# Performance work log

Hardware: AMD Instinct MI355X
Metric: run time of the kernel (lower is better)

## Reference

```python
import jax, jax.numpy as jnp
import numpy as np

N_NODES = 100000


def gcn_conv(x, W, b, src, dst, n):
    # PyG GCNConv: linear transform, add self-loops, symmetric degree norm, scatter-add, bias
    h = x @ W                                      # [n, d_out]
    loop = jnp.arange(n, dtype=src.dtype)
    s = jnp.concatenate([src, loop])               # [E + n]
    d = jnp.concatenate([dst, loop])
    deg = jax.ops.segment_sum(jnp.ones_like(d, dtype=h.dtype), d, num_segments=n)
    dinv = jnp.where(deg > 0, jax.lax.rsqrt(deg), 0.0)
    norm = dinv[s] * dinv[d]                       # [E + n]
    msg = h[s] * norm[:, None]                     # gather + scale
    out = jax.ops.segment_sum(msg, d, num_segments=n)  # scatter-add over targets
    return out + b


def setup_inputs() -> dict:
    key = jax.random.key(0)
    ks = jax.random.split(key, 8)
    n, c_in, hid, c_out = N_NODES, 256, 128, 64
    x = jax.random.normal(ks[0], (n, c_in), dtype=jnp.float32)
    edge_index = jax.random.randint(ks[1], (2, 1600000), 0, n, dtype=jnp.int64)
    s = 0.1
    return {
        "x": x,
        "edge_index": edge_index,
        "W1": jax.random.normal(ks[2], (c_in, hid), dtype=jnp.float32) * s,
        "b1": jnp.zeros((hid,), dtype=jnp.float32),
        "Wmu": jax.random.normal(ks[3], (hid, c_out), dtype=jnp.float32) * s,
        "bmu": jnp.zeros((c_out,), dtype=jnp.float32),
        "Wlv": jax.random.normal(ks[4], (hid, c_out), dtype=jnp.float32) * s,
        "blv": jnp.zeros((c_out,), dtype=jnp.float32),
    }


def reference(x, edge_index, W1, b1, Wmu, bmu, Wlv, blv):
    n = x.shape[0]
    src, dst = edge_index[0], edge_index[1]
    h = jax.nn.relu(gcn_conv(x, W1, b1, src, dst, n))
    mu = gcn_conv(h, Wmu, bmu, src, dst, n)
    logvar = gcn_conv(h, Wlv, blv, src, dst, n)
    return mu, logvar
```

## Files before the change

### kernel.cpp

```cpp
#include <hip/hip_runtime.h>


#define C_IN  256
#define HID   128
#define C_OUT 64
#define NBUCK 1024
#define P1WGS 256

typedef __attribute__((ext_vector_type(8))) short bf16x8;
typedef __attribute__((ext_vector_type(4))) float f32x4;

__device__ inline unsigned short f2bf(float f) {
  unsigned u = __float_as_uint(f);
  unsigned r = u + 0x7FFF + ((u >> 16) & 1);
  return (unsigned short)(r >> 16);
}
__device__ inline float bflo(unsigned v) { return __uint_as_float(v << 16); }
__device__ inline float bfhi(unsigned v) { return __uint_as_float(v & 0xFFFF0000u); }

__global__ __launch_bounds__(256) void k_bin_count(const int* __restrict__ dst,
                                                   int* __restrict__ histmat, int E) {
  __shared__ int h[NBUCK];
  int tid = threadIdx.x;
  for (int i = tid; i < NBUCK; i += 256) h[i] = 0;
  __syncthreads();
  for (int e = blockIdx.x * 256 + tid; e < E; e += P1WGS * 256)
    atomicAdd(&h[dst[e] >> 7], 1);
  __syncthreads();
  for (int i = tid; i < NBUCK; i += 256)
    histmat[blockIdx.x * NBUCK + i] = h[i];
}

__global__ __launch_bounds__(256) void k_col_scan(int* __restrict__ histmat,
                                                  int* __restrict__ bucket_tot) {
  __shared__ int sh[P1WGS];
  int b = blockIdx.x;
  int t = threadIdx.x;
  int v = histmat[t * NBUCK + b];
  sh[t] = v; __syncthreads();
  for (int ofs = 1; ofs < P1WGS; ofs <<= 1) {
    int add = (t >= ofs) ? sh[t - ofs] : 0;
    __syncthreads();
    sh[t] += add;
    __syncthreads();
  }
  histmat[t * NBUCK + b] = sh[t] - v;
  if (t == P1WGS - 1) bucket_tot[b] = sh[t];
}

__global__ void k_bucket_scan(const int* __restrict__ bucket_tot,
                              int* __restrict__ bucket_start, int E) {
  __shared__ int sh[NBUCK];
  int t = threadIdx.x;
  int v = bucket_tot[t];
  sh[t] = v; __syncthreads();
  for (int ofs = 1; ofs < NBUCK; ofs <<= 1) {
    int add = (t >= ofs) ? sh[t - ofs] : 0;
    __syncthreads();
    sh[t] += add;
    __syncthreads();
  }
  bucket_start[t] = sh[t] - v;
  if (t == NBUCK - 1) bucket_start[NBUCK] = E;
}

__global__ __launch_bounds__(256) void k_bin_scatter(const int* __restrict__ src,
                                                     const int* __restrict__ dst,
                                                     const int* __restrict__ histmat,
                                                     const int* __restrict__ bucket_start,
                                                     unsigned* __restrict__ binned, int E) {
  __shared__ int cur[NBUCK];
  int tid = threadIdx.x;
  for (int i = tid; i < NBUCK; i += 256)
    cur[i] = bucket_start[i] + histmat[blockIdx.x * NBUCK + i];
  __syncthreads();
  for (int e = blockIdx.x * 256 + tid; e < E; e += P1WGS * 256) {
    int d = dst[e];
    int pos = atomicAdd(&cur[d >> 7], 1);
    binned[pos] = (unsigned)src[e] | ((unsigned)(d & 127) << 17);
  }
}

__global__ __launch_bounds__(256) void k_bucket_csr(const unsigned* __restrict__ binned,
                                                    const int* __restrict__ bucket_start,
                                                    int* __restrict__ row_start,
                                                    float* __restrict__ dinv,
                                                    int* __restrict__ csr_src,
                                                    int n, int E) {
  __shared__ int h[128], ls[128], c[128];
  int b = blockIdx.x, t = threadIdx.x;
  int start = bucket_start[b], end = bucket_start[b + 1];
  if (t < 128) h[t] = 0;
  __syncthreads();
  for (int e = start + t; e < end; e += 256)
    atomicAdd(&h[binned[e] >> 17], 1);
  __syncthreads();
  if (t < 128) ls[t] = h[t];
  __syncthreads();
  for (int ofs = 1; ofs < 128; ofs <<= 1) {
    int add = (t < 128 && t >= ofs) ? ls[t - ofs] : 0;
    __syncthreads();
    if (t < 128) ls[t] += add;
    __syncthreads();
  }
  if (t < 128) {
    int excl = ls[t] - h[t];
    ls[t] = excl;
    c[t] = excl;
    int node = b * 128 + t;
    if (node < n) {
      row_start[node] = start + excl;
      dinv[node] = rsqrtf((float)h[t] + 1.0f);
    }
  }
  if (b == 0 && t == 0) row_start[n] = E;
  __syncthreads();
  for (int e = start + t; e < end; e += 256) {
    unsigned v = binned[e];
    int pos = start + atomicAdd(&c[v >> 17], 1);
    csr_src[pos] = (int)(v & 0x1FFFF);
  }
}

__global__ void k_prep(const float* __restrict__ W1, const float* __restrict__ Wmu,
                       const float* __restrict__ Wlv,
                       unsigned short* __restrict__ bswz1,
                       unsigned short* __restrict__ bswz2) {
  int idx = blockIdx.x * 256 + threadIdx.x;
  if (idx < 4096) {
    int L = idx & 63, t = (idx >> 6) & 7, s = idx >> 9;
    const float* srcp = W1 + (size_t)(s * 32 + ((L >> 4) << 3)) * 128 + t * 16 + (L & 15);
    unsigned short* dstp = bswz1 + (size_t)idx * 8;
#pragma unroll
    for (int j = 0; j < 8; j++) dstp[j] = f2bf(srcp[(size_t)j * 128]);
  } else if (idx < 6144) {
    int id2 = idx - 4096;
    int L = id2 & 63, t = (id2 >> 6) & 7, s = id2 >> 9;
    int nn = t * 16 + (L & 15);
    int k0 = s * 32 + ((L >> 4) << 3);
    const float* W = (nn < C_OUT) ? (Wmu + nn) : (Wlv + (nn - C_OUT));
    unsigned short* dstp = bswz2 + (size_t)id2 * 8;
#pragma unroll
    for (int j = 0; j < 8; j++) dstp[j] = f2bf(W[(size_t)(k0 + j) * C_OUT]);
  }
}

template <typename AT, int K>
__global__ __launch_bounds__(256) void k_gemm_mfma(const AT* __restrict__ A,
                                                   const unsigned short* __restrict__ bswz,
                                                   unsigned short* __restrict__ C,
                                                   int M) {
  constexpr int NS = K / 32;
  int wave = threadIdx.x >> 6, lane = threadIdx.x & 63;
  int m0 = blockIdx.x * 64 + wave * 16;
  int lrow = lane & 15, lq = lane >> 4;
  int arow = m0 + lrow;
  bool rv = arow < M;
  const AT* ap = A + (size_t)(rv ? arow : 0) * K + lq * 8;

  auto loadA = [&](int s) -> bf16x8 {
    if (sizeof(AT) == 4) {
      const float* af = (const float*)ap + s * 32;
      float4 u0 = rv ? *(const float4*)(af) : float4{0, 0, 0, 0};
      float4 u1 = rv ? *(const float4*)(af + 4) : float4{0, 0, 0, 0};
      union { unsigned short us[8]; bf16x8 v; } tmp;
      tmp.us[0] = f2bf(u0.x); tmp.us[1] = f2bf(u0.y);
      tmp.us[2] = f2bf(u0.z); tmp.us[3] = f2bf(u0.w);
      tmp.us[4] = f2bf(u1.x); tmp.us[5] = f2bf(u1.y);
      tmp.us[6] = f2bf(u1.z); tmp.us[7] = f2bf(u1.w);
      return tmp.v;
    } else {
      const unsigned short* ab = (const unsigned short*)ap + s * 32;
      return rv ? *(const bf16x8*)(ab) : (bf16x8)(short)0;
    }
  };

  f32x4 acc[8];
#pragma unroll
  for (int t = 0; t < 8; t++) acc[t] = (f32x4){0.f, 0.f, 0.f, 0.f};

  bf16x8 a_cur = loadA(0);
  bf16x8 b_cur[8];
#pragma unroll
  for (int t = 0; t < 8; t++)
    b_cur[t] = *(const bf16x8*)(bswz + lane * 8 + t * 512);

#pragma unroll
  for (int s = 0; s < NS; ++s) {
    bf16x8 a_nxt = a_cur;
    bf16x8 b_nxt[8];
    if (s + 1 < NS) {
      a_nxt = loadA(s + 1);
      const unsigned short* bp = bswz + (size_t)(s + 1) * 4096 + lane * 8;
#pragma unroll
      for (int t = 0; t < 8; t++) b_nxt[t] = *(const bf16x8*)(bp + t * 512);
    }
#pragma unroll
    for (int t = 0; t < 8; t++)
      acc[t] = __builtin_amdgcn_mfma_f32_16x16x32_bf16(a_cur, b_cur[t], acc[t], 0, 0, 0);
    a_cur = a_nxt;
    if (s + 1 < NS) {
#pragma unroll
      for (int t = 0; t < 8; t++) b_cur[t] = b_nxt[t];
    }
  }
#pragma unroll
  for (int i = 0; i < 4; i++) {
    int rr = m0 + lq * 4 + i;
    if (rr < M) {
      unsigned short* cp = C + (size_t)rr * 128 + lrow;
#pragma unroll
      for (int t = 0; t < 8; t++) cp[t * 16] = f2bf(acc[t][i]);
    }
  }
}

__device__ inline float rdlane_f(float v, int k) {
  return __uint_as_float(__builtin_amdgcn_readlane(__float_as_uint(v), k));
}

#define AGG_BODY                                                                    \
  int wid = (blockIdx.x * blockDim.x + threadIdx.x) >> 6;                           \
  int lane = threadIdx.x & 63;                                                      \
  if (wid >= n) return;                                                             \
  int rs = row_start[wid], re = row_start[wid + 1];                                 \
  float di = dinv[wid];                                                             \
  float acc0 = 0.f, acc1 = 0.f;                                                     \
  for (int base = rs; base < re + 1; base += 64) {                                  \
    int idx = base + lane;                                                          \
    int sl = wid; float wl = 0.f;                                                   \
    if (idx < re) { sl = csr[idx]; wl = dinv[sl]; }                                 \
    else if (idx == re) { wl = di; }                                 \
    int m = re + 1 - base; if (m > 64) m = 64;                                      \
    int mr = (m + 7) & ~7;                                               \
    for (int k = 0; k < mr; k += 8) {                                               \
      _Pragma("unroll")                                                             \
      for (int j = 0; j < 8; j++) {                                                 \
        int kk = k + j;                                                             \
        int sk = __builtin_amdgcn_readlane(sl, kk);                                 \
        float wk = rdlane_f(wl, kk);                                                \
        unsigned v = *(const unsigned*)(p + (size_t)sk * 128 + 2 * lane);           \
        acc0 += bflo(v) * wk;                                                       \
        acc1 += bfhi(v) * wk;                                                       \
      }                                                                             \
    }                                                                               \
  }                                                                                 \
  acc0 *= di; acc1 *= di;

__global__ __launch_bounds__(256) void k_agg_relu_bf(
    const unsigned short* __restrict__ p, const float* __restrict__ dinv,
    const int* __restrict__ row_start, const int* __restrict__ csr,
    const float* __restrict__ bias, unsigned short* __restrict__ h, int n) {
  AGG_BODY
  float2 bb = *(const float2*)(bias + 2 * lane);
  float r0 = fmaxf(acc0 + bb.x, 0.f);
  float r1 = fmaxf(acc1 + bb.y, 0.f);
  unsigned pk = (unsigned)f2bf(r0) | ((unsigned)f2bf(r1) << 16);
  *(unsigned*)(h + (size_t)wid * 128 + 2 * lane) = pk;
}

__global__ __launch_bounds__(256) void k_agg_out_bf(
    const unsigned short* __restrict__ p, const float* __restrict__ dinv,
    const int* __restrict__ row_start, const int* __restrict__ csr,
    const float* __restrict__ bmu, const float* __restrict__ blv,
    float* __restrict__ out, int n) {
  AGG_BODY
  float2 bb = (lane < 32) ? *(const float2*)(bmu + 2 * lane)
                          : *(const float2*)(blv + 2 * lane - 64);
  float* op = (lane < 32) ? (out + (size_t)wid * C_OUT + 2 * lane)
                          : (out + (size_t)(n + wid) * C_OUT + 2 * lane - 64);
  float2 res = {acc0 + bb.x, acc1 + bb.y};
  *(float2*)op = res;
}

extern "C" void kernel_launch(void* const* d_in, const int* in_sizes, int n_in,
                              void* d_out, int out_size, void* d_ws, size_t ws_size,
                              hipStream_t stream) {
  const float* x   = (const float*)d_in[0];
  const int*   ei  = (const int*)d_in[1];
  const float* W1  = (const float*)d_in[2];
  const float* b1  = (const float*)d_in[3];
  const float* Wmu = (const float*)d_in[4];
  const float* bmu = (const float*)d_in[5];
  const float* Wlv = (const float*)d_in[6];
  const float* blv = (const float*)d_in[7];
  float* out = (float*)d_out;

  const int n = in_sizes[0] / C_IN;
  const int E = in_sizes[1] / 2;
  const int* src = ei;
  const int* dst = ei + E;

  char* w = (char*)d_ws;
  auto alloc = [&](size_t bytes) -> void* {
    void* pp = (void*)w;
    w += (bytes + 255) & ~(size_t)255;
    return pp;
  };
  float*          dinv       = (float*)alloc((size_t)n * 4);
  int*            row_start  = (int*)alloc((size_t)(n + 1) * 4);
  int*            histmat    = (int*)alloc((size_t)P1WGS * NBUCK * 4);
  int*            bucket_tot = (int*)alloc((size_t)NBUCK * 4);
  int*            bucket_st  = (int*)alloc((size_t)(NBUCK + 1) * 4);
  unsigned*       binned     = (unsigned*)alloc((size_t)E * 4);
  int*            csr_src    = (int*)alloc((size_t)E * 4);
  unsigned short* bswz1      = (unsigned short*)alloc((size_t)C_IN * 128 * 2);
  unsigned short* bswz2      = (unsigned short*)alloc((size_t)HID * 128 * 2);
  unsigned short* p1         = (unsigned short*)alloc((size_t)n * 128 * 2);
  unsigned short* hbuf       = (unsigned short*)alloc((size_t)n * 128 * 2);
  unsigned short* p2         = (unsigned short*)alloc((size_t)n * 128 * 2);
  (void)ws_size; (void)n_in; (void)out_size;

  const int TB = 256;
  const int gemm_bks = (n + 63) / 64;
  const int agg_bks = (int)(((size_t)n * 64 + TB - 1) / TB);
  const int nbk_csr = (n + 127) / 128;

  k_bin_count<<<P1WGS, TB, 0, stream>>>(dst, histmat, E);
  k_col_scan<<<NBUCK, TB, 0, stream>>>(histmat, bucket_tot);
  k_bucket_scan<<<1, NBUCK, 0, stream>>>(bucket_tot, bucket_st, E);
  k_bin_scatter<<<P1WGS, TB, 0, stream>>>(src, dst, histmat, bucket_st, binned, E);
  k_bucket_csr<<<nbk_csr, TB, 0, stream>>>(binned, bucket_st, row_start, dinv,
                                           csr_src, n, E);

  k_prep<<<24, 256, 0, stream>>>(W1, Wmu, Wlv, bswz1, bswz2);

  k_gemm_mfma<float, C_IN><<<gemm_bks, TB, 0, stream>>>(x, bswz1, p1, n);
  k_agg_relu_bf<<<agg_bks, TB, 0, stream>>>(p1, dinv, row_start, csr_src, b1, hbuf, n);

  k_gemm_mfma<unsigned short, HID><<<gemm_bks, TB, 0, stream>>>(hbuf, bswz2, p2, n);
  k_agg_out_bf<<<agg_bks, TB, 0, stream>>>(p2, dinv, row_start, csr_src, bmu, blv, out, n);
}
```

Measured before the change: 406.1 us.

## Pre-scale GEMM rows by dinv and aggregate over feature slices

The GEMM epilogue now multiplies each output row by dinv[src] and writes it in a sliced layout of 8 slices with 16 columns each, so the aggregation no longer gathers a per-edge weight. Aggregation is split across 8 slice blocks per node group. Within a wave, each 8-lane group handles one edge and reads a 32-byte slice row, and the partial sums are combined with xor shuffles. The intent is a smaller per-slice gather footprint that stays cache-resident and less readlane/scalar overhead. In exchange, the csr lists and row_start are read eight times and each wave does a reduction.

```diff
diff --git a/kernel.cpp b/kernel.cpp
--- a/kernel.cpp
+++ b/kernel.cpp
@@ -105,7 +105,6 @@
   }
   if (t < 128) {
     int excl = ls[t] - h[t];
-    ls[t] = excl;
     c[t] = excl;
     int node = b * 128 + t;
     if (node < n) {
@@ -148,7 +147,8 @@
 template <typename AT, int K>
 __global__ __launch_bounds__(256) void k_gemm_mfma(const AT* __restrict__ A,
                                                    const unsigned short* __restrict__ bswz,
-                                                   unsigned short* __restrict__ C,
+                                                   const float* __restrict__ dscale,
+                                                   unsigned short* __restrict__ q,
                                                    int M) {
   constexpr int NS = K / 32;
   int wave = threadIdx.x >> 6, lane = threadIdx.x & 63;
@@ -208,69 +208,70 @@
   for (int i = 0; i < 4; i++) {
     int rr = m0 + lq * 4 + i;
     if (rr < M) {
-      unsigned short* cp = C + (size_t)rr * 128 + lrow;
-#pragma unroll
-      for (int t = 0; t < 8; t++) cp[t * 16] = f2bf(acc[t][i]);
-    }
-  }
-}
-
-__device__ inline float rdlane_f(float v, int k) {
-  return __uint_as_float(__builtin_amdgcn_readlane(__float_as_uint(v), k));
-}
-
-#define AGG_BODY                                                                    \
-  int wid = (blockIdx.x * blockDim.x + threadIdx.x) >> 6;                           \
+      float sc = dscale[rr];
+#pragma unroll
+      for (int t = 0; t < 8; t++)
+        q[((size_t)t * M + rr) * 16 + lrow] = f2bf(acc[t][i] * sc);
+    }
+  }
+}
+
+#define AGG_SLICE_BODY                                                              \
+  int slice = blockIdx.x & 7;                                                       \
+  int wave = threadIdx.x >> 6;                                                      \
+  int wid = (blockIdx.x >> 3) * 4 + wave;                                           \
+  if (wid >= n) return;                                                             \
   int lane = threadIdx.x & 63;                                                      \
-  if (wid >= n) return;                                                             \
-  int rs = row_start[wid], re = row_start[wid + 1];                                 \
-  float di = dinv[wid];                                                             \
-  float acc0 = 0.f, acc1 = 0.f;                                                     \
-  for (int base = rs; base < re + 1; base += 64) {                                  \
-    int idx = base + lane;                                                          \
-    int sl = wid; float wl = 0.f;                                                   \
-    if (idx < re) { sl = csr[idx]; wl = dinv[sl]; }                                 \
-    else if (idx == re) { wl = di; }                                 \
-    int m = re + 1 - base; if (m > 64) m = 64;                                      \
-    int mr = (m + 7) & ~7;                                               \
-    for (int k = 0; k < mr; k += 8) {                                               \
-      _Pragma("unroll")                                                             \
-      for (int j = 0; j < 8; j++) {                                                 \
-        int kk = k + j;                                                             \
-        int sk = __builtin_amdgcn_readlane(sl, kk);                                 \
-        float wk = rdlane_f(wl, kk);                                                \
-        unsigned v = *(const unsigned*)(p + (size_t)sk * 128 + 2 * lane);           \
-        acc0 += bflo(v) * wk;                                                       \
-        acc1 += bfhi(v) * wk;                                                       \
-      }                                                                             \
-    }                                                                               \
+  int g = lane >> 3, f = lane & 7;                                                  \
+  int rs = row_start[wid];                                                          \
+  int deg = row_start[wid + 1] - rs;                                                \
+  const unsigned short* qs = q + (size_t)slice * n * 16;                            \
+  float a0 = 0.f, a1 = 0.f;                                                         \
+  for (int t0 = 0; t0 <= deg; t0 += 16) {                                           \
+    int i0 = t0 + g, i1 = t0 + 8 + g;                                               \
+    int s0 = (i0 < deg) ? csr[rs + i0] : wid;                                       \
+    int s1 = (i1 < deg) ? csr[rs + i1] : wid;                                       \
+    unsigned v0 = *(const unsigned*)(qs + (size_t)s0 * 16 + f * 2);                 \
+    unsigned v1 = *(const unsigned*)(qs + (size_t)s1 * 16 + f * 2);                 \
+    if (i0 > deg) v0 = 0;                                                           \
+    if (i1 > deg) v1 = 0;                                                           \
+    a0 += bflo(v0); a1 += bfhi(v0);                                                 \
+    a0 += bflo(v1); a1 += bfhi(v1);                                                 \
   }                                                                                 \
-  acc0 *= di; acc1 *= di;
-
-__global__ __launch_bounds__(256) void k_agg_relu_bf(
-    const unsigned short* __restrict__ p, const float* __restrict__ dinv,
+  a0 += __shfl_xor(a0, 8);  a1 += __shfl_xor(a1, 8);                                \
+  a0 += __shfl_xor(a0, 16); a1 += __shfl_xor(a1, 16);                               \
+  a0 += __shfl_xor(a0, 32); a1 += __shfl_xor(a1, 32);                               \
+  float di = dinv[wid];
+
+__global__ __launch_bounds__(256) void k_agg_relu_sl(
+    const unsigned short* __restrict__ q, const float* __restrict__ dinv,
     const int* __restrict__ row_start, const int* __restrict__ csr,
     const float* __restrict__ bias, unsigned short* __restrict__ h, int n) {
-  AGG_BODY
-  float2 bb = *(const float2*)(bias + 2 * lane);
-  float r0 = fmaxf(acc0 + bb.x, 0.f);
-  float r1 = fmaxf(acc1 + bb.y, 0.f);
-  unsigned pk = (unsigned)f2bf(r0) | ((unsigned)f2bf(r1) << 16);
-  *(unsigned*)(h + (size_t)wid * 128 + 2 * lane) = pk;
-}
-
-__global__ __launch_bounds__(256) void k_agg_out_bf(
-    const unsigned short* __restrict__ p, const float* __restrict__ dinv,
+  AGG_SLICE_BODY
+  if (g == 0) {
+    float2 bb = *(const float2*)(bias + slice * 16 + 2 * f);
+    float r0 = fmaxf(a0 * di + bb.x, 0.f);
+    float r1 = fmaxf(a1 * di + bb.y, 0.f);
+    unsigned pk = (unsigned)f2bf(r0) | ((unsigned)f2bf(r1) << 16);
+    *(unsigned*)(h + (size_t)wid * 128 + slice * 16 + 2 * f) = pk;
+  }
+}
+
+__global__ __launch_bounds__(256) void k_agg_out_sl(
+    const unsigned short* __restrict__ q, const float* __restrict__ dinv,
     const int* __restrict__ row_start, const int* __restrict__ csr,
     const float* __restrict__ bmu, const float* __restrict__ blv,
     float* __restrict__ out, int n) {
-  AGG_BODY
-  float2 bb = (lane < 32) ? *(const float2*)(bmu + 2 * lane)
-                          : *(const float2*)(blv + 2 * lane - 64);
-  float* op = (lane < 32) ? (out + (size_t)wid * C_OUT + 2 * lane)
-                          : (out + (size_t)(n + wid) * C_OUT + 2 * lane - 64);
-  float2 res = {acc0 + bb.x, acc1 + bb.y};
-  *(float2*)op = res;
+  AGG_SLICE_BODY
+  if (g == 0) {
+    int c0 = (slice & 3) * 16 + 2 * f;
+    float2 bb = (slice < 4) ? *(const float2*)(bmu + c0)
+                            : *(const float2*)(blv + c0);
+    float* op = (slice < 4) ? (out + (size_t)wid * C_OUT + c0)
+                            : (out + (size_t)(n + wid) * C_OUT + c0);
+    float2 res = {a0 * di + bb.x, a1 * di + bb.y};
+    *(float2*)op = res;
+  }
 }
 
 extern "C" void kernel_launch(void* const* d_in, const int* in_sizes, int n_in,
@@ -306,14 +307,14 @@
   int*            csr_src    = (int*)alloc((size_t)E * 4);
   unsigned short* bswz1      = (unsigned short*)alloc((size_t)C_IN * 128 * 2);
   unsigned short* bswz2      = (unsigned short*)alloc((size_t)HID * 128 * 2);
-  unsigned short* p1         = (unsigned short*)alloc((size_t)n * 128 * 2);
+  unsigned short* q1         = (unsigned short*)alloc((size_t)n * 128 * 2);
   unsigned short* hbuf       = (unsigned short*)alloc((size_t)n * 128 * 2);
-  unsigned short* p2         = (unsigned short*)alloc((size_t)n * 128 * 2);
+  unsigned short* q2         = (unsigned short*)alloc((size_t)n * 128 * 2);
   (void)ws_size; (void)n_in; (void)out_size;
 
   const int TB = 256;
   const int gemm_bks = (n + 63) / 64;
-  const int agg_bks = (int)(((size_t)n * 64 + TB - 1) / TB);
+  const int agg_bks = ((n + 3) / 4) * 8;
   const int nbk_csr = (n + 127) / 128;
 
   k_bin_count<<<P1WGS, TB, 0, stream>>>(dst, histmat, E);
@@ -325,9 +326,9 @@
 
   k_prep<<<24, 256, 0, stream>>>(W1, Wmu, Wlv, bswz1, bswz2);
 
-  k_gemm_mfma<float, C_IN><<<gemm_bks, TB, 0, stream>>>(x, bswz1, p1, n);
-  k_agg_relu_bf<<<agg_bks, TB, 0, stream>>>(p1, dinv, row_start, csr_src, b1, hbuf, n);
-
-  k_gemm_mfma<unsigned short, HID><<<gemm_bks, TB, 0, stream>>>(hbuf, bswz2, p2, n);
-  k_agg_out_bf<<<agg_bks, TB, 0, stream>>>(p2, dinv, row_start, csr_src, bmu, blv, out, n);
-}
+  k_gemm_mfma<float, C_IN><<<gemm_bks, TB, 0, stream>>>(x, bswz1, dinv, q1, n);
+  k_agg_relu_sl<<<agg_bks, TB, 0, stream>>>(q1, dinv, row_start, csr_src, b1, hbuf, n);
+
+  k_gemm_mfma<unsigned short, HID><<<gemm_bks, TB, 0, stream>>>(hbuf, bswz2, dinv, q2, n);
+  k_agg_out_sl<<<agg_bks, TB, 0, stream>>>(q2, dinv, row_start, csr_src, bmu, blv, out, n);
+}
```

Measured after the change: 712.5 us. 1.75x slower.
